# Kernel optimization log

Measured on AMD Instinct MI355X. Metric: run time of the kernel, lower is better.

Reference implementation:

```python
import jax, jax.numpy as jnp
import numpy as np

B, H, W, Q, E, M, K, WIN = 4, 192, 192, 160, 96, 96, 4, 7
NO_ELECTRON_WEIGHT = 0.1


def _bce_logits(x, z):
    # binary_cross_entropy_with_logits, elementwise: softplus(x) - x*z
    return jnp.logaddexp(0.0, x) - x * z


def setup_inputs() -> dict:
    key = jax.random.key(0)
    ks = jax.random.split(key, 11)
    is_electron_logit = jax.random.normal(ks[0], (B * Q,), jnp.float32)
    true_segmap = jax.random.uniform(ks[1], (B, H, W, E), jnp.float32)
    binary_mask_logits = jax.random.normal(ks[2], (B, H, W, Q), jnp.float32)
    portion_logits = jax.random.normal(ks[3], (B, H, W, Q), jnp.float32)
    # keep incidence points away from borders so the 7x7 window stays in-bounds
    incidence_points = jax.random.uniform(ks[4], (B, E, 2), jnp.float32) * (H - 8) + 4.0
    positions = jax.random.uniform(ks[5], (B, Q, 2), jnp.float32) * H
    a = jax.random.normal(ks[6], (B, Q, 3), jnp.float32)
    l00 = jax.nn.softplus(a[..., 0]) + 0.1
    l11 = jax.nn.softplus(a[..., 2]) + 0.1
    l10 = 0.5 * a[..., 1]
    zero = jnp.zeros_like(l00)
    chol = jnp.stack([jnp.stack([l00, zero], -1), jnp.stack([l10, l11], -1)], -2)  # [B,Q,2,2] lower-tri
    occupancy_logits = jax.random.normal(ks[7], (B, H, W, K), jnp.float32)
    occupancy_true = jax.random.randint(ks[8], (B, H, W), 0, K, jnp.int32)
    qkeys = jax.random.split(ks[9], B)
    matched_q = jnp.stack([jax.random.permutation(k, Q)[:M] for k in qkeys]).astype(jnp.int32)
    ekeys = jax.random.split(ks[10], B)
    matched_e = jnp.stack([jax.random.permutation(k, E) for k in ekeys]).astype(jnp.int32)
    return dict(is_electron_logit=is_electron_logit, true_segmap=true_segmap,
                binary_mask_logits=binary_mask_logits, portion_logits=portion_logits,
                incidence_points=incidence_points, positions=positions, chol=chol,
                occupancy_logits=occupancy_logits, occupancy_true=occupancy_true,
                matched_q=matched_q, matched_e=matched_e)


def reference(is_electron_logit, true_segmap, binary_mask_logits, portion_logits,
              incidence_points, positions, chol, occupancy_logits, occupancy_true,
              matched_q, matched_e):
    # ---- class loss (weighted BCE over flat per-query logits) ----
    labels = jnp.zeros((B * Q,), is_electron_logit.dtype)
    glob = (jnp.arange(B)[:, None] * Q + matched_q).reshape(-1)
    labels = labels.at[glob].set(1.0)
    weights = jnp.where(labels > 0, 1.0, NO_ELECTRON_WEIGHT).astype(is_electron_logit.dtype)
    class_loss = jnp.mean(weights * _bce_logits(is_electron_logit, labels))

    # ---- reorder segmentation maps to matched order (_reorder_segmentation_map) ----
    true_r = jnp.take_along_axis(true_segmap, matched_e[:, None, None, :], axis=3)        # [B,H,W,M]
    bin_r = jnp.take_along_axis(binary_mask_logits, matched_q[:, None, None, :], axis=3)  # [B,H,W,M]
    por_r = jnp.take_along_axis(portion_logits, matched_q[:, None, None, :], axis=3)      # [B,H,W,M]

    # ---- mask BCE on 7x7 windows around floor(matched incidence point) ----
    pts_r = jnp.take_along_axis(incidence_points, matched_e[..., None], axis=1)  # [B,M,2]
    pix = jnp.floor(pts_r).astype(jnp.int32)
    half = WIN // 2
    dr = jnp.arange(-half, half + 1)
    rows = pix[..., 0][:, :, None, None] + dr[None, None, :, None]  # [B,M,7,1]
    cols = pix[..., 1][:, :, None, None] + dr[None, None, None, :]  # [B,M,1,7]
    bi = jnp.arange(B)[:, None, None, None]
    mi = jnp.arange(M)[None, :, None, None]
    tv = true_r[bi, rows, cols, mi]  # [B,M,7,7]
    lg = bin_r[bi, rows, cols, mi]
    bce_loss = jnp.mean(_bce_logits(lg, tv))

    # ---- dice loss (softmax over matched-electron dim) ----
    portion = jax.nn.softmax(por_r, axis=-1)
    num = jnp.sum(2.0 * true_r * portion, axis=(1, 2, 3))
    den = jnp.sum(true_r + portion, axis=(1, 2, 3))
    dice_loss = jnp.mean(1.0 - (num + 1.0) / (den + 1.0))

    # ---- distance NLL (2D MVN with lower-tri scale) ----
    centers_r = jnp.take_along_axis(positions, matched_q[..., None], axis=1)       # [B,M,2]
    chol_r = jnp.take_along_axis(chol, matched_q[..., None, None], axis=1)         # [B,M,2,2]
    d = pts_r - centers_r
    z0 = d[..., 0] / chol_r[..., 0, 0]
    z1 = (d[..., 1] - chol_r[..., 1, 0] * z0) / chol_r[..., 1, 1]
    nll = 0.5 * (z0 * z0 + z1 * z1) + jnp.log(2.0 * jnp.pi) \
          + jnp.log(chol_r[..., 0, 0]) + jnp.log(chol_r[..., 1, 1])
    nll = jnp.where(jnp.isinf(nll), 1e7, nll)
    nll_loss = jnp.mean(nll)

    # ---- occupancy loss (per-pixel electron-count cross-entropy) ----
    logp = jax.nn.log_softmax(occupancy_logits, axis=-1)
    occ_loss = -jnp.mean(jnp.take_along_axis(logp, occupancy_true[..., None], axis=-1))

    # loss_weights all 1.0 (defaults); dot(weights, terms)
    return class_loss + bce_loss + dice_loss + nll_loss + occ_loss
```

## Files before the change

kernel.cpp:

```cpp
#include <hip/hip_runtime.h>
#include <math.h>

#define B_ 4
#define H_ 192
#define W_ 192
#define Q_ 160
#define E_ 96
#define M_ 96
#define HW_ (H_ * W_)
#define NPIX_ (B_ * HW_)
#define NDICE 1024
#define NTSUM 1024
#define NSMALL 962
#define NBUCKET 64
#define WS_NUM0 4
#define WS_TS0  260
#define WS_TOTAL 516

template <int CTRL, int RMASK>
__device__ inline float dpp_add_step(float x) {
    int v = __builtin_amdgcn_update_dpp(0, __float_as_int(x), CTRL, RMASK, 0xF, false);
    return x + __int_as_float(v);
}
__device__ inline float wave_sum63(float x) {
    x = dpp_add_step<0x111, 0xF>(x);
    x = dpp_add_step<0x112, 0xF>(x);
    x = dpp_add_step<0x114, 0xF>(x);
    x = dpp_add_step<0x118, 0xF>(x);
    x = dpp_add_step<0x142, 0xA>(x);
    x = dpp_add_step<0x143, 0xC>(x);
    return x;
}

__device__ inline float waveSumAll(float v) {
    for (int m = 32; m > 0; m >>= 1) v += __shfl_xor(v, m, 64);
    return v;
}

__device__ inline float softplusf(float x) {
    return fmaxf(x, 0.f) + log1pf(__expf(-fabsf(x)));
}

__global__ __launch_bounds__(256) void fused_kernel(
    const float* __restrict__ logit,
    const float* __restrict__ trueseg,
    const float* __restrict__ binlog,
    const float* __restrict__ por,
    const float* __restrict__ inc,
    const float* __restrict__ pos,
    const float* __restrict__ chol,
    const float* __restrict__ occlog,
    const int* __restrict__ occtrue,
    const int* __restrict__ mqall,
    const int* __restrict__ meall,
    float* __restrict__ ws)
{
    __shared__ float red[256];
    __shared__ float sN[4][B_];
    __shared__ float lab[B_ * Q_];
    const int tid  = threadIdx.x;
    const int lane = tid & 63;
    const int wid  = tid >> 6;
    const int blk  = blockIdx.x;

    if (blk < NDICE) {
        const int wave = blk * 4 + wid;
        const bool hi = lane < 32;
        for (int b = 0; b < B_; ++b) {
            const int* mq = mqall + b * M_;
            const int* me = meall + b * M_;
            const int mqa = mq[lane];
            const int mea = me[lane];
            int mqb = 0, meb = 0;
            if (hi) { mqb = mq[64 + lane]; meb = me[64 + lane]; }
            const float* porb = por + (size_t)b * HW_ * Q_;
            const float* trb  = trueseg + (size_t)b * HW_ * E_;
            float an = 0.f;
            #pragma unroll 3
            for (int it = 0; it < 9; ++it) {
                const int p = wave + it * 4096;
                const float* pr = porb + (size_t)p * Q_;
                const float* tr = trb  + (size_t)p * E_;
                float p0 = pr[mqa];
                float t0 = tr[mea];
                float e1 = 0.f, se1 = 0.f;
                if (hi) {
                    float p1 = pr[mqb];
                    float t1 = tr[meb];
                    e1 = __expf(p1);
                    se1 = t1 * e1;
                }
                float e0 = __expf(p0);
                float s  = wave_sum63(e0 + e1);
                float se = wave_sum63(t0 * e0 + se1);
                an += __fdividef(se, s);
            }
            if (lane == 63) sN[wid][b] = an;
        }
        __syncthreads();
        if (tid < B_) {
            float tot = sN[0][tid] + sN[1][tid] + sN[2][tid] + sN[3][tid];
            atomicAdd(&ws[WS_NUM0 + (blk & (NBUCKET - 1)) * 4 + tid], 2.f * tot);
        }
    } else if (blk < NDICE + NTSUM) {
        const int j = blk - NDICE;
        const int b = j >> 8;
        const float4* t4 = (const float4*)(trueseg + (size_t)b * HW_ * E_);
        const int NF4 = HW_ * E_ / 4;
        float a = 0.f;
        for (int idx = (j & 255) * 256 + tid; idx < NF4; idx += 256 * 256) {
            float4 v = t4[idx];
            a += (v.x + v.y) + (v.z + v.w);
        }
        a = wave_sum63(a);
        if (lane == 63) sN[wid][0] = a;
        __syncthreads();
        if (tid == 0) {
            float tot = sN[0][0] + sN[1][0] + sN[2][0] + sN[3][0];
            atomicAdd(&ws[WS_TS0 + (blk & (NBUCKET - 1)) * 4 + b], tot);
        }
    } else {
        const int s = blk - (NDICE + NTSUM);
        float acc = 0.f;
        if (s == 0) {
            for (int i = tid; i < B_ * Q_; i += 256) lab[i] = 0.f;
            __syncthreads();
            for (int i = tid; i < B_ * M_; i += 256) {
                int b = i / M_;
                lab[b * Q_ + mqall[i]] = 1.f;
            }
            __syncthreads();
            for (int i = tid; i < B_ * Q_; i += 256) {
                float x = logit[i];
                float z = lab[i];
                float w = z > 0.f ? 1.f : 0.1f;
                acc += w * (softplusf(x) - x * z);
            }
            red[tid] = acc; __syncthreads();
            for (int st = 128; st > 0; st >>= 1) { if (tid < st) red[tid] += red[tid + st]; __syncthreads(); }
            if (tid == 0) ws[0] = red[0];
        } else if (s == 1) {
            for (int i = tid; i < B_ * M_; i += 256) {
                int b = i / M_;
                int qi = mqall[i];
                int ei = meall[i];
                float px = inc[(b * E_ + ei) * 2 + 0];
                float py = inc[(b * E_ + ei) * 2 + 1];
                float cx = pos[(b * Q_ + qi) * 2 + 0];
                float cy = pos[(b * Q_ + qi) * 2 + 1];
                const float* ch = chol + (size_t)(b * Q_ + qi) * 4;
                float l00 = ch[0], l10 = ch[2], l11 = ch[3];
                float d0 = px - cx, d1 = py - cy;
                float z0 = d0 / l00;
                float z1 = (d1 - l10 * z0) / l11;
                float nll = 0.5f * (z0 * z0 + z1 * z1) + 1.837877066409345f
                            + logf(l00) + logf(l11);
                if (isinf(nll)) nll = 1e7f;
                acc += nll;
            }
            red[tid] = acc; __syncthreads();
            for (int st = 128; st > 0; st >>= 1) { if (tid < st) red[tid] += red[tid + st]; __syncthreads(); }
            if (tid == 0) ws[2] = red[0];
        } else if (s < 386) {
            int idx = s - 2;
            int b = idx / M_;
            int ei = meall[idx];
            int qi = mqall[idx];
            float px = inc[(b * E_ + ei) * 2 + 0];
            float py = inc[(b * E_ + ei) * 2 + 1];
            int r0 = (int)floorf(px) - 3;
            int c0 = (int)floorf(py) - 3;
            if (tid < 49) {
                int rr = r0 + tid / 7;
                int cc = c0 + tid % 7;
                size_t pix = ((size_t)b * H_ + rr) * W_ + cc;
                float tv = trueseg[pix * E_ + ei];
                float lg = binlog[pix * Q_ + qi];
                acc = softplusf(lg) - lg * tv;
            }
            red[tid] = acc; __syncthreads();
            for (int st = 128; st > 0; st >>= 1) { if (tid < st) red[tid] += red[tid + st]; __syncthreads(); }
            if (tid == 0) atomicAdd(&ws[1], red[0]);
        } else {
            int p = (s - 386) * 256 + tid;
            if (p < NPIX_) {
                float4 v = *(const float4*)(occlog + (size_t)p * 4);
                int lb = occtrue[p];
                float m = fmaxf(fmaxf(v.x, v.y), fmaxf(v.z, v.w));
                float lse = m + __logf(__expf(v.x - m) + __expf(v.y - m) +
                                       __expf(v.z - m) + __expf(v.w - m));
                float xs = lb == 0 ? v.x : (lb == 1 ? v.y : (lb == 2 ? v.z : v.w));
                acc = lse - xs;
            }
            red[tid] = acc; __syncthreads();
            for (int st = 128; st > 0; st >>= 1) { if (tid < st) red[tid] += red[tid + st]; __syncthreads(); }
            if (tid == 0) atomicAdd(&ws[3], red[0]);
        }
    }
}

__global__ __launch_bounds__(64) void final_kernel(const float* __restrict__ ws,
                                                   float* __restrict__ out)
{
    const int lane = threadIdx.x;
    float n[B_], t[B_];
    for (int b = 0; b < B_; ++b) {
        n[b] = waveSumAll(ws[WS_NUM0 + lane * 4 + b]);
        t[b] = waveSumAll(ws[WS_TS0  + lane * 4 + b]);
    }
    if (lane == 0) {
        float class_l = ws[0] * (1.f / (B_ * Q_));
        float bce_l   = ws[1] * (1.f / (B_ * M_ * 49));
        float nll_l   = ws[2] * (1.f / (B_ * M_));
        float occ_l   = ws[3] * (1.f / NPIX_);
        float dice = 0.f;
        for (int b = 0; b < B_; ++b)
            dice += 1.f - (n[b] + 1.f) / (t[b] + (float)HW_ + 1.f);
        dice *= (1.f / B_);
        out[0] = class_l + bce_l + nll_l + occ_l + dice;
    }
}

extern "C" void kernel_launch(void* const* d_in, const int* in_sizes, int n_in,
                              void* d_out, int out_size, void* d_ws, size_t ws_size,
                              hipStream_t stream) {
    const float* logit   = (const float*)d_in[0];
    const float* trueseg = (const float*)d_in[1];
    const float* binlog  = (const float*)d_in[2];
    const float* por     = (const float*)d_in[3];
    const float* inc     = (const float*)d_in[4];
    const float* pos     = (const float*)d_in[5];
    const float* chol    = (const float*)d_in[6];
    const float* occlog  = (const float*)d_in[7];
    const int*   occtrue = (const int*)d_in[8];
    const int*   mq      = (const int*)d_in[9];
    const int*   me      = (const int*)d_in[10];
    float* out = (float*)d_out;
    float* ws  = (float*)d_ws;

    (void)hipMemsetAsync(d_ws, 0, WS_TOTAL * sizeof(float), stream);

    hipLaunchKernelGGL(fused_kernel, dim3(NDICE + NTSUM + NSMALL), dim3(256), 0, stream,
                       logit, trueseg, binlog, por, inc, pos, chol, occlog, occtrue,
                       mq, me, ws);
    hipLaunchKernelGGL(final_kernel, dim3(1), dim3(64), 0, stream, ws, out);
}
```

Baseline: 250.3 us.

## Stage dice tiles through LDS and fuse true-segmap sum into dice pass

Dice blocks now each own one batch and copy 16-pixel tiles of portion logits and true segmap into shared memory with coalesced float4 loads. The next tile is prefetched into registers while the current one is processed. The scattered matched-index gathers then read from LDS instead of global memory. The separate blocks that re-read the whole true segmap for its sum are removed, and the sum is taken from the gathered values. This relies on matched_e being a full permutation of E, and it adds two block barriers per tile.

```diff
diff --git a/kernel.cpp b/kernel.cpp
--- a/kernel.cpp
+++ b/kernel.cpp
@@ -9,8 +9,10 @@
 #define M_ 96
 #define HW_ (H_ * W_)
 #define NPIX_ (B_ * HW_)
+#define TPIX 16
+#define NTILE_B 2304
+#define TILES_PER_BLK 9
 #define NDICE 1024
-#define NTSUM 1024
 #define NSMALL 962
 #define NBUCKET 64
 #define WS_NUM0 4
@@ -40,6 +42,11 @@
 __device__ inline float softplusf(float x) {
     return fmaxf(x, 0.f) + log1pf(__expf(-fabsf(x)));
 }
+
+#define POR_BYTES (TPIX * Q_ * 4)
+#define TRU_BYTES (TPIX * E_ * 4)
+#define TILE_BYTES (POR_BYTES + TRU_BYTES)
+#define POR_F (TPIX * Q_)
 
 __global__ __launch_bounds__(256) void fused_kernel(
     const float* __restrict__ logit,
@@ -55,8 +62,9 @@
     const int* __restrict__ meall,
     float* __restrict__ ws)
 {
+    __shared__ float4 tilebuf[TILE_BYTES / 16];
     __shared__ float red[256];
-    __shared__ float sN[4][B_];
+    __shared__ float sA[4], sT[4];
     __shared__ float lab[B_ * Q_];
     const int tid  = threadIdx.x;
     const int lane = tid & 63;
@@ -64,63 +72,78 @@
     const int blk  = blockIdx.x;
 
     if (blk < NDICE) {
-        const int wave = blk * 4 + wid;
+        const int b = blk >> 8;
+        const int slot = blk & 255;
         const bool hi = lane < 32;
-        for (int b = 0; b < B_; ++b) {
-            const int* mq = mqall + b * M_;
-            const int* me = meall + b * M_;
-            const int mqa = mq[lane];
-            const int mea = me[lane];
-            int mqb = 0, meb = 0;
-            if (hi) { mqb = mq[64 + lane]; meb = me[64 + lane]; }
-            const float* porb = por + (size_t)b * HW_ * Q_;
-            const float* trb  = trueseg + (size_t)b * HW_ * E_;
-            float an = 0.f;
-            #pragma unroll 3
-            for (int it = 0; it < 9; ++it) {
-                const int p = wave + it * 4096;
-                const float* pr = porb + (size_t)p * Q_;
-                const float* tr = trb  + (size_t)p * E_;
-                float p0 = pr[mqa];
-                float t0 = tr[mea];
-                float e1 = 0.f, se1 = 0.f;
+        const int* mq = mqall + b * M_;
+        const int* me = meall + b * M_;
+        const int mqa = mq[lane];
+        const int mea = me[lane];
+        int mqb = 0, meb = 0;
+        if (hi) { mqb = mq[64 + lane]; meb = me[64 + lane]; }
+        const char* porb = (const char*)(por + (size_t)b * HW_ * Q_);
+        const char* trb  = (const char*)(trueseg + (size_t)b * HW_ * E_);
+
+        float4 pf[4];
+        auto load_tile = [&](int t) {
+            const int p0 = (slot + t * 256) * TPIX;
+            const char* gp = porb + (size_t)p0 * (Q_ * 4);
+            const char* gt = trb  + (size_t)p0 * (E_ * 4);
+            #pragma unroll
+            for (int i = 0; i < 4; ++i) {
+                int off = tid * 16 + i * 4096;
+                pf[i] = (off < POR_BYTES)
+                        ? *(const float4*)(gp + off)
+                        : *(const float4*)(gt + (off - POR_BYTES));
+            }
+        };
+        auto store_tile = [&]() {
+            #pragma unroll
+            for (int i = 0; i < 4; ++i) tilebuf[tid + i * 256] = pf[i];
+        };
+
+        const float* pl = (const float*)tilebuf;
+        const float* tl = (const float*)tilebuf + POR_F;
+        float an = 0.f;
+        float at = 0.f;
+
+        load_tile(0);
+        for (int t = 0; t < TILES_PER_BLK; ++t) {
+            store_tile();
+            __syncthreads();
+            if (t + 1 < TILES_PER_BLK) load_tile(t + 1);
+            #pragma unroll
+            for (int k = 0; k < 4; ++k) {
+                const int pix = wid * 4 + k;
+                float p0v = pl[pix * Q_ + mqa];
+                float t0  = tl[pix * E_ + mea];
+                float e1 = 0.f, se1 = 0.f, t1 = 0.f;
                 if (hi) {
-                    float p1 = pr[mqb];
-                    float t1 = tr[meb];
+                    float p1 = pl[pix * Q_ + mqb];
+                    t1 = tl[pix * E_ + meb];
                     e1 = __expf(p1);
                     se1 = t1 * e1;
                 }
-                float e0 = __expf(p0);
+                float e0 = __expf(p0v);
                 float s  = wave_sum63(e0 + e1);
                 float se = wave_sum63(t0 * e0 + se1);
                 an += __fdividef(se, s);
-            }
-            if (lane == 63) sN[wid][b] = an;
+                at += t0 + t1;
+            }
+            __syncthreads();
         }
-        __syncthreads();
-        if (tid < B_) {
-            float tot = sN[0][tid] + sN[1][tid] + sN[2][tid] + sN[3][tid];
-            atomicAdd(&ws[WS_NUM0 + (blk & (NBUCKET - 1)) * 4 + tid], 2.f * tot);
-        }
-    } else if (blk < NDICE + NTSUM) {
-        const int j = blk - NDICE;
-        const int b = j >> 8;
-        const float4* t4 = (const float4*)(trueseg + (size_t)b * HW_ * E_);
-        const int NF4 = HW_ * E_ / 4;
-        float a = 0.f;
-        for (int idx = (j & 255) * 256 + tid; idx < NF4; idx += 256 * 256) {
-            float4 v = t4[idx];
-            a += (v.x + v.y) + (v.z + v.w);
-        }
-        a = wave_sum63(a);
-        if (lane == 63) sN[wid][0] = a;
+        float atr = wave_sum63(at);
+        if (lane == 63) { sA[wid] = an; sT[wid] = atr; }
         __syncthreads();
         if (tid == 0) {
-            float tot = sN[0][0] + sN[1][0] + sN[2][0] + sN[3][0];
-            atomicAdd(&ws[WS_TS0 + (blk & (NBUCKET - 1)) * 4 + b], tot);
+            float num = sA[0] + sA[1] + sA[2] + sA[3];
+            float ts  = sT[0] + sT[1] + sT[2] + sT[3];
+            int bucket = blk & (NBUCKET - 1);
+            atomicAdd(&ws[WS_NUM0 + bucket * 4 + b], 2.f * num);
+            atomicAdd(&ws[WS_TS0  + bucket * 4 + b], ts);
         }
     } else {
-        const int s = blk - (NDICE + NTSUM);
+        const int s = blk - NDICE;
         float acc = 0.f;
         if (s == 0) {
             for (int i = tid; i < B_ * Q_; i += 256) lab[i] = 0.f;
@@ -240,7 +263,7 @@
 
     (void)hipMemsetAsync(d_ws, 0, WS_TOTAL * sizeof(float), stream);
 
-    hipLaunchKernelGGL(fused_kernel, dim3(NDICE + NTSUM + NSMALL), dim3(256), 0, stream,
+    hipLaunchKernelGGL(fused_kernel, dim3(NDICE + NSMALL), dim3(256), 0, stream,
                        logit, trueseg, binlog, por, inc, pos, chol, occlog, occtrue,
                        mq, me, ws);
     hipLaunchKernelGGL(final_kernel, dim3(1), dim3(64), 0, stream, ws, out);
```

Measured after the change: 259.7 us. 3.7% more time.

## Fold segmap total into dice gather and software-pipeline loads across batches

Applied to the files above, without the earlier changes.

Drops the separate blocks that streamed the whole true_segmap to get its per-batch sum. The sum is now taken from the values the dice gather already loads. This is exact only because matched_e is a full permutation of the electron axis, so every channel is visited once. The dice loop now handles all four batches per iteration and prefetches the next pixel's gathered values, giving more loads in flight at the cost of more registers.

```diff
diff --git a/kernel.cpp b/kernel.cpp
--- a/kernel.cpp
+++ b/kernel.cpp
@@ -10,7 +10,6 @@
 #define HW_ (H_ * W_)
 #define NPIX_ (B_ * HW_)
 #define NDICE 1024
-#define NTSUM 1024
 #define NSMALL 962
 #define NBUCKET 64
 #define WS_NUM0 4
@@ -18,11 +17,11 @@
 #define WS_TOTAL 516
 
 template <int CTRL, int RMASK>
-__device__ inline float dpp_add_step(float x) {
+__device__ __forceinline__ float dpp_add_step(float x) {
     int v = __builtin_amdgcn_update_dpp(0, __float_as_int(x), CTRL, RMASK, 0xF, false);
     return x + __int_as_float(v);
 }
-__device__ inline float wave_sum63(float x) {
+__device__ __forceinline__ float wave_sum63(float x) {
     x = dpp_add_step<0x111, 0xF>(x);
     x = dpp_add_step<0x112, 0xF>(x);
     x = dpp_add_step<0x114, 0xF>(x);
@@ -32,14 +31,40 @@
     return x;
 }
 
-__device__ inline float waveSumAll(float v) {
+__device__ __forceinline__ float waveSumAll(float v) {
     for (int m = 32; m > 0; m >>= 1) v += __shfl_xor(v, m, 64);
     return v;
 }
 
-__device__ inline float softplusf(float x) {
+__device__ __forceinline__ float softplusf(float x) {
     return fmaxf(x, 0.f) + log1pf(__expf(-fabsf(x)));
 }
+
+#define LOAD_POS(P, P0, T0, P1, T1) do {                                   \
+    const size_t _p = (size_t)(P);                                         \
+    const float* _r0 = pb0 + _p * Q_; const float* _r1 = pb1 + _p * Q_;    \
+    const float* _r2 = pb2 + _p * Q_; const float* _r3 = pb3 + _p * Q_;    \
+    const float* _s0 = tb0 + _p * E_; const float* _s1 = tb1 + _p * E_;    \
+    const float* _s2 = tb2 + _p * E_; const float* _s3 = tb3 + _p * E_;    \
+    P0.x = _r0[mqa0]; P0.y = _r1[mqa1]; P0.z = _r2[mqa2]; P0.w = _r3[mqa3];\
+    T0.x = _s0[mea0]; T0.y = _s1[mea1]; T0.z = _s2[mea2]; T0.w = _s3[mea3];\
+    if (hi) {                                                              \
+        P1.x = _r0[mqb0]; P1.y = _r1[mqb1]; P1.z = _r2[mqb2]; P1.w = _r3[mqb3]; \
+        T1.x = _s0[meb0]; T1.y = _s1[meb1]; T1.z = _s2[meb2]; T1.w = _s3[meb3]; \
+    } else {                                                               \
+        P1.x = P1.y = P1.z = P1.w = 0.f;                                   \
+        T1.x = T1.y = T1.z = T1.w = 0.f;                                   \
+    }                                                                      \
+} while (0)
+
+#define DICE_ONE(p0c, t0c, p1c, t1c, anref, atref) do {                    \
+    float _e1 = hi ? __expf(p1c) : 0.f;                                    \
+    float _e0 = __expf(p0c);                                               \
+    float _s  = wave_sum63(_e0 + _e1);                                     \
+    float _se = wave_sum63(fmaf(t0c, _e0, t1c * _e1));                     \
+    anref += __fdividef(_se, _s);                                          \
+    atref += t0c + t1c;                                                    \
+} while (0)
 
 __global__ __launch_bounds__(256) void fused_kernel(
     const float* __restrict__ logit,
@@ -56,8 +81,8 @@
     float* __restrict__ ws)
 {
     __shared__ float red[256];
-    __shared__ float sN[4][B_];
     __shared__ float lab[B_ * Q_];
+    __shared__ float sA[4][B_], sT[4][B_];
     const int tid  = threadIdx.x;
     const int lane = tid & 63;
     const int wid  = tid >> 6;
@@ -66,61 +91,57 @@
     if (blk < NDICE) {
         const int wave = blk * 4 + wid;
         const bool hi = lane < 32;
-        for (int b = 0; b < B_; ++b) {
-            const int* mq = mqall + b * M_;
-            const int* me = meall + b * M_;
-            const int mqa = mq[lane];
-            const int mea = me[lane];
-            int mqb = 0, meb = 0;
-            if (hi) { mqb = mq[64 + lane]; meb = me[64 + lane]; }
-            const float* porb = por + (size_t)b * HW_ * Q_;
-            const float* trb  = trueseg + (size_t)b * HW_ * E_;
-            float an = 0.f;
-            #pragma unroll 3
-            for (int it = 0; it < 9; ++it) {
-                const int p = wave + it * 4096;
-                const float* pr = porb + (size_t)p * Q_;
-                const float* tr = trb  + (size_t)p * E_;
-                float p0 = pr[mqa];
-                float t0 = tr[mea];
-                float e1 = 0.f, se1 = 0.f;
-                if (hi) {
-                    float p1 = pr[mqb];
-                    float t1 = tr[meb];
-                    e1 = __expf(p1);
-                    se1 = t1 * e1;
-                }
-                float e0 = __expf(p0);
-                float s  = wave_sum63(e0 + e1);
-                float se = wave_sum63(t0 * e0 + se1);
-                an += __fdividef(se, s);
-            }
-            if (lane == 63) sN[wid][b] = an;
+        const int mqa0 = mqall[0 * M_ + lane], mqa1 = mqall[1 * M_ + lane],
+                  mqa2 = mqall[2 * M_ + lane], mqa3 = mqall[3 * M_ + lane];
+        const int mea0 = meall[0 * M_ + lane], mea1 = meall[1 * M_ + lane],
+                  mea2 = meall[2 * M_ + lane], mea3 = meall[3 * M_ + lane];
+        int mqb0 = 0, mqb1 = 0, mqb2 = 0, mqb3 = 0;
+        int meb0 = 0, meb1 = 0, meb2 = 0, meb3 = 0;
+        if (hi) {
+            mqb0 = mqall[0 * M_ + 64 + lane]; mqb1 = mqall[1 * M_ + 64 + lane];
+            mqb2 = mqall[2 * M_ + 64 + lane]; mqb3 = mqall[3 * M_ + 64 + lane];
+            meb0 = meall[0 * M_ + 64 + lane]; meb1 = meall[1 * M_ + 64 + lane];
+            meb2 = meall[2 * M_ + 64 + lane]; meb3 = meall[3 * M_ + 64 + lane];
+        }
+        const float* pb0 = por;
+        const float* pb1 = por + (size_t)1 * HW_ * Q_;
+        const float* pb2 = por + (size_t)2 * HW_ * Q_;
+        const float* pb3 = por + (size_t)3 * HW_ * Q_;
+        const float* tb0 = trueseg;
+        const float* tb1 = trueseg + (size_t)1 * HW_ * E_;
+        const float* tb2 = trueseg + (size_t)2 * HW_ * E_;
+        const float* tb3 = trueseg + (size_t)3 * HW_ * E_;
+
+        float4 an = {0.f, 0.f, 0.f, 0.f};
+        float4 at = {0.f, 0.f, 0.f, 0.f};
+
+        float4 cP0, cT0, cP1, cT1, nP0, nT0, nP1, nT1;
+        LOAD_POS(wave, cP0, cT0, cP1, cT1);
+        #pragma unroll
+        for (int it = 0; it < 9; ++it) {
+            if (it < 8) LOAD_POS(wave + (it + 1) * 4096, nP0, nT0, nP1, nT1);
+            DICE_ONE(cP0.x, cT0.x, cP1.x, cT1.x, an.x, at.x);
+            DICE_ONE(cP0.y, cT0.y, cP1.y, cT1.y, an.y, at.y);
+            DICE_ONE(cP0.z, cT0.z, cP1.z, cT1.z, an.z, at.z);
+            DICE_ONE(cP0.w, cT0.w, cP1.w, cT1.w, an.w, at.w);
+            cP0 = nP0; cT0 = nT0; cP1 = nP1; cT1 = nT1;
+        }
+        at.x = wave_sum63(at.x); at.y = wave_sum63(at.y);
+        at.z = wave_sum63(at.z); at.w = wave_sum63(at.w);
+        if (lane == 63) {
+            sA[wid][0] = an.x; sA[wid][1] = an.y; sA[wid][2] = an.z; sA[wid][3] = an.w;
+            sT[wid][0] = at.x; sT[wid][1] = at.y; sT[wid][2] = at.z; sT[wid][3] = at.w;
         }
         __syncthreads();
         if (tid < B_) {
-            float tot = sN[0][tid] + sN[1][tid] + sN[2][tid] + sN[3][tid];
-            atomicAdd(&ws[WS_NUM0 + (blk & (NBUCKET - 1)) * 4 + tid], 2.f * tot);
-        }
-    } else if (blk < NDICE + NTSUM) {
-        const int j = blk - NDICE;
-        const int b = j >> 8;
-        const float4* t4 = (const float4*)(trueseg + (size_t)b * HW_ * E_);
-        const int NF4 = HW_ * E_ / 4;
-        float a = 0.f;
-        for (int idx = (j & 255) * 256 + tid; idx < NF4; idx += 256 * 256) {
-            float4 v = t4[idx];
-            a += (v.x + v.y) + (v.z + v.w);
-        }
-        a = wave_sum63(a);
-        if (lane == 63) sN[wid][0] = a;
-        __syncthreads();
-        if (tid == 0) {
-            float tot = sN[0][0] + sN[1][0] + sN[2][0] + sN[3][0];
-            atomicAdd(&ws[WS_TS0 + (blk & (NBUCKET - 1)) * 4 + b], tot);
+            float num = sA[0][tid] + sA[1][tid] + sA[2][tid] + sA[3][tid];
+            float ts  = sT[0][tid] + sT[1][tid] + sT[2][tid] + sT[3][tid];
+            int bucket = blk & (NBUCKET - 1);
+            atomicAdd(&ws[WS_NUM0 + bucket * 4 + tid], 2.f * num);
+            atomicAdd(&ws[WS_TS0  + bucket * 4 + tid], ts);
         }
     } else {
-        const int s = blk - (NDICE + NTSUM);
+        const int s = blk - NDICE;
         float acc = 0.f;
         if (s == 0) {
             for (int i = tid; i < B_ * Q_; i += 256) lab[i] = 0.f;
@@ -240,7 +261,7 @@
 
     (void)hipMemsetAsync(d_ws, 0, WS_TOTAL * sizeof(float), stream);
 
-    hipLaunchKernelGGL(fused_kernel, dim3(NDICE + NTSUM + NSMALL), dim3(256), 0, stream,
+    hipLaunchKernelGGL(fused_kernel, dim3(NDICE + NSMALL), dim3(256), 0, stream,
                        logit, trueseg, binlog, por, inc, pos, chol, occlog, occtrue,
                        mq, me, ws);
     hipLaunchKernelGGL(final_kernel, dim3(1), dim3(64), 0, stream, ws, out);
```

New measurement: 252.0 us. No clear change (+0.7%).
